# Kernel tuning notes

Hardware: AMD Instinct MI355X
Metric: run time of the kernel (lower is better)

Reference implementation:

```python
import jax, jax.numpy as jnp
import numpy as np

U, I, G = 200000, 100000, 10000
D = 64
LAYERS = 3
E_HG = 3_000_000
E_GI = 2_000_000
B = 8192


def setup_inputs() -> dict:
    key = jax.random.key(0)
    ks = jax.random.split(key, 20)
    n_hg = U + G
    n_gi = G + I
    xav = lambda k, shape: (jax.random.normal(k, shape, jnp.float32) * 0.05)
    inp = {
        "user_inputs": jax.random.randint(ks[0], (B,), 0, U),
        "pos_groups": jax.random.randint(ks[1], (B,), 0, G),
        "neg_groups": jax.random.randint(ks[2], (B,), 0, G),
        # hypergraph propagation matrix (normalized-adjacency-like values)
        "hg_rows": jax.random.randint(ks[3], (E_HG,), 0, n_hg),
        "hg_cols": jax.random.randint(ks[4], (E_HG,), 0, n_hg),
        "hg_vals": jax.random.uniform(ks[5], (E_HG,), jnp.float32) / 16.0,
        # group-item bipartite graph (one LightGCN hop)
        "gi_rows": jax.random.randint(ks[6], (E_GI,), 0, n_gi),
        "gi_cols": jax.random.randint(ks[7], (E_GI,), 0, n_gi),
        "gi_vals": jax.random.uniform(ks[8], (E_GI,), jnp.float32) / 16.0,
        # dense group-group overlap matrix
        "gg_graph": jax.random.uniform(ks[9], (G, G), jnp.float32) / float(G),
        # learned parameters
        "user_emb": xav(ks[10], (U, D)),
        "item_emb": xav(ks[11], (I, D)),
        "group_emb": xav(ks[12], (G, D)),
        "hyper_w": xav(ks[13], (D, 1)),
        "hyper_b": jnp.zeros((1,), jnp.float32),
        "lightgcn_w": xav(ks[14], (D, 1)),
        "lightgcn_b": jnp.zeros((1,), jnp.float32),
        "overlap_w": xav(ks[15], (D, 1)),
        "overlap_b": jnp.zeros((1,), jnp.float32),
    }
    return inp


def spmm(rows, cols, vals, x, n):
    # sparse(n,n) @ x : gather cols, scale, scatter-add into rows
    return jax.ops.segment_sum(vals[:, None] * x[cols], rows, num_segments=n)


def reference(user_inputs, pos_groups, neg_groups,
              hg_rows, hg_cols, hg_vals,
              gi_rows, gi_cols, gi_vals,
              gg_graph,
              user_emb, item_emb, group_emb,
              hyper_w, hyper_b, lightgcn_w, lightgcn_b, overlap_w, overlap_b):
    # --- hypergraph branch: layered SpMM + mean over (layers+1) views ---
    hg = jnp.concatenate([user_emb, group_emb], axis=0)  # [U+G, D]
    acc = hg
    cur = hg
    for _ in range(LAYERS):
        cur = spmm(hg_rows, hg_cols, hg_vals, cur, U + G)
        acc = acc + cur
    hg_mean = acc / float(LAYERS + 1)
    hg_users = hg_mean[:U]   # [U, D]
    hg_groups = hg_mean[U:]  # [G, D]

    # --- lightgcn branch: one SpMM hop over group-item graph ---
    gi = jnp.concatenate([group_emb, item_emb], axis=0)  # [G+I, D]
    gi = spmm(gi_rows, gi_cols, gi_vals, gi, G + I)
    gi_groups = gi[:G]

    # --- overlap branch: dense group-group propagation ---
    gg = gg_graph @ group_emb  # [G, D]

    # --- gated multi-view fusion ---
    sig = jax.nn.sigmoid
    hyper_coef = sig(hg_groups @ hyper_w + hyper_b)      # [G, 1]
    lightgcn_coef = sig(gi_groups @ lightgcn_w + lightgcn_b)
    overlap_coef = sig(gg @ overlap_w + overlap_b)
    groups_final = hyper_coef * hg_groups + lightgcn_coef * gi_groups + overlap_coef * gg
    users_final = hg_users

    return (users_final[user_inputs], groups_final[pos_groups], groups_final[neg_groups],
            user_emb[user_inputs], group_emb[pos_groups], group_emb[neg_groups])
```

## Files before the change

kernel.cpp:

```cpp
#include <hip/hip_runtime.h>
#include <hip/hip_bf16.h>

#define U_N 200000
#define I_N 100000
#define G_N 10000
#define B_N 8192
#define NHG (U_N + G_N)
#define GG_K 10000
#define GG_STRIPES 157
#define GG_SPLIT 8
#define GG_SC_TOT 79
#define GG_KC4 316
#define ROWSTR 136

#define BUCK_SHIFT 8
#define BUCK_ROWS 256
#define NBUCK 821
#define ACHUNK 12288

typedef __attribute__((ext_vector_type(8))) short bf16x8;
typedef __attribute__((ext_vector_type(4))) float f32x4;
typedef __attribute__((ext_vector_type(8))) float f32x8;
typedef __attribute__((ext_vector_type(8))) unsigned short us8;

static __device__ __forceinline__ float sigmoidf_(float x) {
    return 1.0f / (1.0f + __expf(-x));
}

static __device__ __forceinline__ unsigned bfc(float x) {
    unsigned u = __float_as_uint(x);
    return (u + 0x7fffu + ((u >> 16) & 1u)) >> 16;
}
static __device__ __forceinline__ float bsf(unsigned short u) {
    return __uint_as_float((unsigned)u << 16);
}

__global__ void k_phase1(const float* __restrict__ ge, short* __restrict__ Bfrag,
                         int* __restrict__ cursor, int cap, int bfB) {
    int bx = blockIdx.x;
    if (bx < bfB) {
        int t = bx * 256 + threadIdx.x;
        int l = t & 63;
        int ct = (t >> 6) & 3;
        int kc = t >> 8;
        int j = ct * 16 + (l & 15);
        int kb = kc * 32 + (l >> 4) * 8;
        bf16x8 pack;
#pragma unroll
        for (int e = 0; e < 8; ++e) {
            int k = kb + e;
            float f = (k < GG_K) ? ge[(size_t)k * 64 + j] : 0.f;
            pack[e] = (short)bfc(f);
        }
        *(bf16x8*)(Bfrag + (size_t)t * 8) = pack;
        return;
    }
    int b = (bx - bfB) * 256 + threadIdx.x;
    if (b < NBUCK) cursor[b] = b * cap;
}


static __device__ __forceinline__ void bscatter_body(const int* __restrict__ rows,
                                                     const int* __restrict__ cols,
                                                     const float* __restrict__ vals,
                                                     int* __restrict__ cursor,
                                                     int2* __restrict__ bpair,
                                                     int nE, int cap, int blk) {
    __shared__ int h[NBUCK];
    __shared__ int base[NBUCK];
    for (int i = threadIdx.x; i < NBUCK; i += 256) h[i] = 0;
    __syncthreads();
    int s = blk * ACHUNK;
    int end = s + ACHUNK; if (end > nE) end = nE;
    for (int e = s + threadIdx.x; e < end; e += 256)
        atomicAdd(&h[rows[e] >> BUCK_SHIFT], 1);
    __syncthreads();
    for (int i = threadIdx.x; i < NBUCK; i += 256) {
        int c = h[i];
        base[i] = c ? atomicAdd(&cursor[i], c) : 0;
        h[i] = 0;
    }
    __syncthreads();
    for (int e = s + threadIdx.x; e < end; e += 256) {
        int r = rows[e];
        int b = r >> BUCK_SHIFT;
        int pos = base[b] + atomicAdd(&h[b], 1);
        if (pos < (b + 1) * cap)
            bpair[pos] = make_int2(((r & (BUCK_ROWS - 1)) << 24) | cols[e],
                                   __float_as_int(vals[e]));
    }
}

static __device__ __forceinline__ void gg_mfma_body(const float* __restrict__ A,
                                                    const short* __restrict__ Bfrag,
                                                    float* __restrict__ part, int blk) {
    __shared__ short lds_a[64 * ROWSTR];
    const int stripe = blk % GG_STRIPES;
    const int ks = blk / GG_STRIPES;
    const int sc0 = ks * 10;
    const int sc1 = (ks == 7) ? GG_SC_TOT : sc0 + 10;
    const int tid = threadIdx.x;
    const int w = tid >> 6, l = tid & 63;
    const int r0w = stripe * 64 + w * 16;
    const int srow = tid >> 5;
    const int scol = (tid & 31) * 4;
    f32x4 acc0 = {0.f, 0.f, 0.f, 0.f}, acc1 = acc0, acc2 = acc0, acc3 = acc0;
    for (int sc = sc0; sc < sc1; ++sc) {
        __syncthreads();
#pragma unroll
        for (int pass = 0; pass < 8; ++pass) {
            int rl = pass * 8 + srow;
            int rg = stripe * 64 + rl; if (rg > GG_K - 1) rg = GG_K - 1;
            int kg = sc * 128 + scol;
            float4 a = {0.f, 0.f, 0.f, 0.f};
            if (kg < GG_K) a = *(const float4*)(A + (size_t)rg * GG_K + kg);
            ushort4 o;
            o.x = (unsigned short)bfc(a.x); o.y = (unsigned short)bfc(a.y);
            o.z = (unsigned short)bfc(a.z); o.w = (unsigned short)bfc(a.w);
            *(ushort4*)(lds_a + rl * ROWSTR + scol) = o;
        }
        __syncthreads();
#pragma unroll
        for (int q = 0; q < 4; ++q) {
            int kc = sc * 4 + q;
            bf16x8 af = *(const bf16x8*)(lds_a + (w * 16 + (l & 15)) * ROWSTR
                                         + q * 32 + (l >> 4) * 8);
            const bf16x8* bp = (const bf16x8*)(Bfrag + (size_t)kc * 4 * 64 * 8);
            bf16x8 b0 = bp[0 * 64 + l];
            bf16x8 b1 = bp[1 * 64 + l];
            bf16x8 b2 = bp[2 * 64 + l];
            bf16x8 b3 = bp[3 * 64 + l];
            acc0 = __builtin_amdgcn_mfma_f32_16x16x32_bf16(af, b0, acc0, 0, 0, 0);
            acc1 = __builtin_amdgcn_mfma_f32_16x16x32_bf16(af, b1, acc1, 0, 0, 0);
            acc2 = __builtin_amdgcn_mfma_f32_16x16x32_bf16(af, b2, acc2, 0, 0, 0);
            acc3 = __builtin_amdgcn_mfma_f32_16x16x32_bf16(af, b3, acc3, 0, 0, 0);
        }
    }
    float* po = part + (size_t)ks * GG_K * 64;
    const int orow0 = r0w + (l >> 4) * 4;
    const int ocol = l & 15;
#pragma unroll
    for (int reg = 0; reg < 4; ++reg) {
        int orow = orow0 + reg;
        if (orow < GG_K) {
            float* q = po + (size_t)orow * 64 + ocol;
            q[0]  = acc0[reg];
            q[16] = acc1[reg];
            q[32] = acc2[reg];
            q[48] = acc3[reg];
        }
    }
}

__global__ __launch_bounds__(256) void k_phase2(
    const int* __restrict__ rows, const int* __restrict__ cols,
    const float* __restrict__ vals, int* __restrict__ cursor,
    int2* __restrict__ bpair, int nE, int cap,
    const float* __restrict__ A, const short* __restrict__ Bfrag,
    float* __restrict__ part,
    const float4* __restrict__ ue4, const float4* __restrict__ ge4,
    ushort4* __restrict__ out4, const int* __restrict__ ui,
    float* __restrict__ ua, float* __restrict__ grp_acc, float* __restrict__ gi_out,
    int bsB, int ggB, int cvtB, int uaB, int gaB) {
    int bx = blockIdx.x;
    if (bx < bsB) { bscatter_body(rows, cols, vals, cursor, bpair, nE, cap, bx); return; }
    bx -= bsB;
    if (bx < ggB) { gg_mfma_body(A, Bfrag, part, bx); return; }
    bx -= ggB;
    if (bx < cvtB) {
        int i = bx * 256 + threadIdx.x;
        float4 f = (i < U_N * 16) ? ue4[i] : ge4[i - U_N * 16];
        ushort4 o;
        o.x = (unsigned short)bfc(f.x);
        o.y = (unsigned short)bfc(f.y);
        o.z = (unsigned short)bfc(f.z);
        o.w = (unsigned short)bfc(f.w);
        out4[i] = o;
        return;
    }
    bx -= cvtB;
    if (bx < uaB) {
        int idx = bx * 256 + threadIdx.x;
        int b = idx >> 6, d = idx & 63;
        ua[idx] = ((const float*)ue4)[(size_t)ui[b] * 64 + d];
        return;
    }
    bx -= uaB;
    if (bx < gaB) {
        int idx = bx * 256 + threadIdx.x;
        grp_acc[idx] = ((const float*)ge4)[idx];
        return;
    }
    bx -= gaB;
    int idx = bx * 256 + threadIdx.x;
    gi_out[idx] = 0.f;
}


static __device__ __forceinline__ void bcsr_body(const int* __restrict__ cursor,
                                                 const int2* __restrict__ bpair,
                                                 int2* __restrict__ ep,
                                                 int* __restrict__ rp, int* __restrict__ cnt,
                                                 int cap, int b) {
    __shared__ int hist[256];
    __shared__ int sc[256];
    const int tid = threadIdx.x;
    const int s = b * cap;
    int e_ = cursor[b];
    if (e_ > s + cap) e_ = s + cap;
    hist[tid] = 0;
    __syncthreads();
    for (int i = s + tid; i < e_; i += 256)
        atomicAdd(&hist[((unsigned)bpair[i].x) >> 24], 1);
    __syncthreads();
    int v = hist[tid];
    sc[tid] = v;
    __syncthreads();
    for (int off = 1; off < 256; off <<= 1) {
        int t = (tid >= off) ? sc[tid - off] : 0;
        __syncthreads();
        if (tid >= off) sc[tid] += t;
        __syncthreads();
    }
    int excl = sc[tid] - v;
    int gr = (b << BUCK_SHIFT) + tid;
    if (gr < NHG) { rp[gr] = s + excl; cnt[gr] = v; }
    hist[tid] = excl;
    __syncthreads();
    for (int i = s + tid; i < e_; i += 256) {
        int2 p = bpair[i];
        unsigned pk = (unsigned)p.x;
        int pos = atomicAdd(&hist[pk >> 24], 1);
        ep[s + pos] = make_int2((int)(pk & 0xFFFFFFu), p.y);
    }
}

static __device__ __forceinline__ void gi_body(const int* __restrict__ rows,
                                               const int* __restrict__ cols,
                                               const float* __restrict__ vals,
                                               const float* __restrict__ ge,
                                               const float* __restrict__ ie,
                                               float* __restrict__ out, int nE,
                                               int blk, int nblk) {
    int lane = threadIdx.x & 63;
    long wslot = (long)blk * 4 + (threadIdx.x >> 6);
    const long nslots = (long)nblk * 4;
    for (long base = wslot * 64; base < nE; base += nslots * 64) {
        long e = base + lane;
        int r = (e < nE) ? rows[e] : 0x7fffffff;
        bool ok = (r < G_N);
        int c = 0;
        float v = 0.f;
        if (ok) { c = cols[e]; v = vals[e]; }
        unsigned long long mask = __ballot(ok);
        while (mask) {
            int srcl = __ffsll(mask) - 1;
            mask &= mask - 1;
            int rr = __shfl(r, srcl, 64);
            int cc = __shfl(c, srcl, 64);
            float vv = __shfl(v, srcl, 64);
            const float* sp = (cc < G_N) ? (ge + (size_t)cc * 64) : (ie + (size_t)(cc - G_N) * 64);
            atomicAdd(&out[(size_t)rr * 64 + lane], vv * sp[lane]);
        }
    }
}

__global__ __launch_bounds__(256) void k_phase3(const int* __restrict__ cursor,
                                                const int2* __restrict__ bpair,
                                                int2* __restrict__ ep,
                                                int* __restrict__ rp, int* __restrict__ cnt,
                                                int cap,
                                                const int* __restrict__ grows,
                                                const int* __restrict__ gcols,
                                                const float* __restrict__ gvals,
                                                const float* __restrict__ ge,
                                                const float* __restrict__ ie,
                                                float* __restrict__ gi_out, int gnE, int giB) {
    if (blockIdx.x < NBUCK)
        bcsr_body(cursor, bpair, ep, rp, cnt, cap, blockIdx.x);
    else
        gi_body(grows, gcols, gvals, ge, ie, gi_out, gnE, blockIdx.x - NBUCK, giB);
}


static __device__ __forceinline__ void spmm_row8(const int2* __restrict__ ep, int s, int n,
                                                 const us8* __restrict__ x16,
                                                 int sub, f32x8& acc) {
#pragma unroll
    for (int t = 0; t < 8; ++t) acc[t] = 0.f;
    for (int i = 0; i < n; i += 8) {
        int2 e[8];
#pragma unroll
        for (int j = 0; j < 8; ++j) {
            int k = i + j;
            int kk = (k < n) ? k : n - 1;
            e[j] = ep[s + kk];
            if (k >= n) { e[j].y = 0; e[j].x = 0; }
        }
        us8 xv[8];
#pragma unroll
        for (int j = 0; j < 8; ++j)
            xv[j] = x16[(size_t)e[j].x * 8 + sub];
#pragma unroll
        for (int j = 0; j < 8; ++j) {
            float v = __int_as_float(e[j].y);
#pragma unroll
            for (int t = 0; t < 8; ++t) acc[t] += v * bsf(xv[j][t]);
        }
    }
}

__global__ void k_spmm8(const int* __restrict__ rp, const int* __restrict__ cnt,
                        const int2* __restrict__ ep, const us8* __restrict__ x16,
                        us8* __restrict__ out16, float* __restrict__ grp_acc,
                        const int* __restrict__ ui, float* __restrict__ usr_acc,
                        int spmmBlocks) {
    if (blockIdx.x >= spmmBlocks) {
        int idx = (blockIdx.x - spmmBlocks) * 256 + threadIdx.x;
        int b = idx >> 3, d = idx & 7;
        us8 u = x16[(size_t)ui[b] * 8 + d];
        f32x8* g = (f32x8*)usr_acc + ((size_t)b * 8 + d);
        f32x8 t = *g;
#pragma unroll
        for (int j = 0; j < 8; ++j) t[j] += bsf(u[j]);
        *g = t;
        return;
    }
    int wid = threadIdx.x >> 6;
    int lane = threadIdx.x & 63;
    int slot = lane >> 3, sub = lane & 7;
    int r = blockIdx.x * 32 + wid * 8 + slot;
    bool active = (r < NHG);
    int rr = active ? r : NHG - 1;
    int s = rp[rr];
    int n = active ? cnt[rr] : 0;
    f32x8 a;
    spmm_row8(ep, s, n, x16, sub, a);
    if (active) {
        us8 o;
#pragma unroll
        for (int j = 0; j < 8; ++j) o[j] = (unsigned short)bfc(a[j]);
        out16[(size_t)r * 8 + sub] = o;
        if (r >= U_N) {
            f32x8* g = (f32x8*)grp_acc + ((size_t)(r - U_N) * 8 + sub);
            f32x8 t = *g;
#pragma unroll
            for (int j = 0; j < 8; ++j) t[j] += a[j];
            *g = t;
        }
    }
}

__global__ void k_spmm8_final(const int* __restrict__ rp, const int* __restrict__ cnt,
                              const int2* __restrict__ ep, const us8* __restrict__ x16,
                              const int* __restrict__ ui,
                              float* __restrict__ grp_acc, float* __restrict__ usr_acc,
                              int taskBlocks) {
    if (blockIdx.x >= taskBlocks) {
        int idx = (blockIdx.x - taskBlocks) * 256 + threadIdx.x;
        int b = idx >> 3, d = idx & 7;
        us8 u = x16[(size_t)ui[b] * 8 + d];
        f32x8* g = (f32x8*)usr_acc + ((size_t)b * 8 + d);
        f32x8 t = *g;
#pragma unroll
        for (int j = 0; j < 8; ++j) t[j] += bsf(u[j]);
        *g = t;
        return;
    }
    int wid = threadIdx.x >> 6;
    int lane = threadIdx.x & 63;
    int slot = lane >> 3, sub = lane & 7;
    int t = blockIdx.x * 32 + wid * 8 + slot;
    bool active = (t < G_N + B_N);
    int tt = active ? t : 0;
    int r = (tt < G_N) ? (U_N + tt) : ui[tt - G_N];
    int s = rp[r];
    int n = active ? cnt[r] : 0;
    f32x8 a;
    spmm_row8(ep, s, n, x16, sub, a);
    if (active) {
        f32x8* g = (tt < G_N) ? ((f32x8*)grp_acc + ((size_t)tt * 8 + sub))
                              : ((f32x8*)usr_acc + ((size_t)(tt - G_N) * 8 + sub));
        f32x8 v = *g;
#pragma unroll
        for (int j = 0; j < 8; ++j) v[j] += a[j];
        *g = v;
    }
}


__global__ void k_gather_fin(const int* __restrict__ ui, const int* __restrict__ pg,
                             const int* __restrict__ ng, const float* __restrict__ ua,
                             const float* __restrict__ ga, const float* __restrict__ gi_out,
                             const float* __restrict__ gg_part,
                             const float* __restrict__ hw, const float* __restrict__ hb,
                             const float* __restrict__ lw, const float* __restrict__ lb,
                             const float* __restrict__ ow, const float* __restrict__ ob,
                             const float* __restrict__ ue, const float* __restrict__ ge,
                             float* __restrict__ out) {
    int wid = threadIdx.x >> 6, lane = threadIdx.x & 63;
    int b = blockIdx.x * 4 + wid;
    const int S = B_N * 64;
    int u = ui[b], p = pg[b], q = ng[b];
    int idx = b * 64 + lane;
    out[idx]         = ua[idx] * 0.25f;
    out[3 * S + idx] = ue[(size_t)u * 64 + lane];
    out[4 * S + idx] = ge[(size_t)p * 64 + lane];
    out[5 * S + idx] = ge[(size_t)q * 64 + lane];
    const size_t SS = (size_t)G_N * 64;
    float hwv = hw[lane], lwv = lw[lane], owv = ow[lane];
    float hb0 = hb[0], lb0 = lb[0], ob0 = ob[0];
#pragma unroll
    for (int which = 0; which < 2; ++which) {
        int g = which ? q : p;
        size_t o = (size_t)g * 64 + lane;
        float hgv = ga[o] * 0.25f;
        float giv = gi_out[o];
        float ggv = 0.f;
#pragma unroll
        for (int k = 0; k < GG_SPLIT; ++k) ggv += gg_part[k * SS + o];
        float d1 = hgv * hwv, d2 = giv * lwv, d3 = ggv * owv;
#pragma unroll
        for (int off2 = 32; off2; off2 >>= 1) {
            d1 += __shfl_xor(d1, off2, 64);
            d2 += __shfl_xor(d2, off2, 64);
            d3 += __shfl_xor(d3, off2, 64);
        }
        float val = sigmoidf_(d1 + hb0) * hgv + sigmoidf_(d2 + lb0) * giv
                  + sigmoidf_(d3 + ob0) * ggv;
        out[(which ? 2 * S : S) + idx] = val;
    }
}

extern "C" void kernel_launch(void* const* d_in, const int* in_sizes, int n_in,
                              void* d_out, int out_size, void* d_ws, size_t ws_size,
                              hipStream_t stream) {
    const int*   ui        = (const int*)d_in[0];
    const int*   pg        = (const int*)d_in[1];
    const int*   ng        = (const int*)d_in[2];
    const int*   hg_rows   = (const int*)d_in[3];
    const int*   hg_cols   = (const int*)d_in[4];
    const float* hg_vals   = (const float*)d_in[5];
    const int*   gi_rows   = (const int*)d_in[6];
    const int*   gi_cols   = (const int*)d_in[7];
    const float* gi_vals   = (const float*)d_in[8];
    const float* gg_graph  = (const float*)d_in[9];
    const float* user_emb  = (const float*)d_in[10];
    const float* item_emb  = (const float*)d_in[11];
    const float* group_emb = (const float*)d_in[12];
    const float* hyper_w   = (const float*)d_in[13];
    const float* hyper_b   = (const float*)d_in[14];
    const float* lgcn_w    = (const float*)d_in[15];
    const float* lgcn_b    = (const float*)d_in[16];
    const float* ovl_w     = (const float*)d_in[17];
    const float* ovl_b     = (const float*)d_in[18];
    const int E_HG = in_sizes[3];
    const int E_GI = in_sizes[6];

    const int nblkA = (E_HG + ACHUNK - 1) / ACHUNK;
    int cap = (E_HG + NBUCK - 1) / NBUCK;
    cap = cap + cap / 4 + 64;
    cap = (cap + 63) & ~63;

    char* ws = (char*)d_ws;
    size_t off = 0;
    auto alloc = [&](size_t bytes) -> char* {
        char* p = ws + off;
        off += (bytes + 255) & ~(size_t)255;
        return p;
    };
    int*   cursor  = (int*)alloc((size_t)NBUCK * 4);
    int2*  bpair   = (int2*)alloc((size_t)NBUCK * cap * 8);
    int2*  ep      = (int2*)alloc((size_t)NBUCK * cap * 8 + 1024);
    int*   rp      = (int*)alloc((size_t)NHG * 4);
    int*   cnt     = (int*)alloc((size_t)NHG * 4);
    __hip_bfloat16* curA = (__hip_bfloat16*)alloc((size_t)NHG * 64 * 2);
    __hip_bfloat16* curB = (__hip_bfloat16*)alloc((size_t)NHG * 64 * 2);
    float* grp_acc = (float*)alloc((size_t)G_N * 64 * 4);
    float* gi_out  = (float*)alloc((size_t)G_N * 64 * 4);
    float* usr_acc = (float*)alloc((size_t)B_N * 64 * 4);
    short* Bfrag   = (short*)alloc((size_t)GG_KC4 * 4 * 64 * 8 * 2);
    float* gg_part = (float*)alloc((size_t)GG_SPLIT * GG_K * 64 * 4);
    (void)ws_size; (void)n_in; (void)out_size;

    k_phase1<<<GG_KC4 + 4, 256, 0, stream>>>(group_emb, Bfrag, cursor, cap, GG_KC4);

    const int ggB  = GG_STRIPES * GG_SPLIT;
    const int cvtB = (NHG * 16) / 256;
    const int uaB  = (B_N * 64) / 256;
    const int gaB  = (G_N * 64) / 256;
    const int gzB  = (G_N * 64) / 256;
    k_phase2<<<nblkA + ggB + cvtB + uaB + gaB + gzB, 256, 0, stream>>>(
        hg_rows, hg_cols, hg_vals, cursor, bpair, E_HG, cap,
        gg_graph, Bfrag, gg_part,
        (const float4*)user_emb, (const float4*)group_emb, (ushort4*)curB, ui,
        usr_acc, grp_acc, gi_out, nblkA, ggB, cvtB, uaB, gaB);

    const int giB = 2048;
    k_phase3<<<NBUCK + giB, 256, 0, stream>>>(cursor, bpair, ep, rp, cnt, cap,
                                              gi_rows, gi_cols, gi_vals,
                                              group_emb, item_emb, gi_out, E_GI, giB);

    const int spmmB = (NHG + 31) / 32;
    const int uaExt = (B_N * 8) / 256;

    k_spmm8<<<spmmB, 256, 0, stream>>>(rp, cnt, ep, (const us8*)curB,
                                       (us8*)curA, grp_acc, nullptr, nullptr, spmmB);
    k_spmm8<<<spmmB + uaExt, 256, 0, stream>>>(rp, cnt, ep, (const us8*)curA,
                                               (us8*)curB, grp_acc, ui, usr_acc, spmmB);
    const int taskB = (G_N + B_N + 31) / 32;
    k_spmm8_final<<<taskB + uaExt, 256, 0, stream>>>(rp, cnt, ep, (const us8*)curB, ui,
                                                     grp_acc, usr_acc, taskB);

    k_gather_fin<<<B_N / 4, 256, 0, stream>>>(ui, pg, ng, usr_acc, grp_acc, gi_out, gg_part,
                                              hyper_w, hyper_b, lgcn_w, lgcn_b, ovl_w, ovl_b,
                                              user_emb, group_emb, (float*)d_out);
}
```

Before: 395.1 us.

## Move group-item SpMM into phase2, split GEMM K finer, prefetch A tiles

The group-item SpMM blocks move out of phase3 and into the phase2 launch, so they run alongside the bucket scatter and the dense GEMM. Phase3 now does only the CSR build, and zeroing gi_out moves earlier into phase1 so it is done before phase2 adds into it. The dense gg GEMM splits K into 16 pieces instead of 8, giving more blocks, and it prefetches the next A tile into registers while the MFMAs run on the current one. The cost is twice the partial-sum buffer and reduction work in the final gather, plus higher register pressure from the prefetch.

```diff
diff --git a/kernel.cpp b/kernel.cpp
--- a/kernel.cpp
+++ b/kernel.cpp
@@ -8,7 +8,7 @@
 #define NHG (U_N + G_N)
 #define GG_K 10000
 #define GG_STRIPES 157
-#define GG_SPLIT 8
+#define GG_SPLIT 16
 #define GG_SC_TOT 79
 #define GG_KC4 316
 #define ROWSTR 136
@@ -36,7 +36,8 @@
 }
 
 __global__ void k_phase1(const float* __restrict__ ge, short* __restrict__ Bfrag,
-                         int* __restrict__ cursor, int cap, int bfB) {
+                         float* __restrict__ gi_out, int* __restrict__ cursor,
+                         int cap, int bfB, int gzB) {
     int bx = blockIdx.x;
     if (bx < bfB) {
         int t = bx * 256 + threadIdx.x;
@@ -55,7 +56,14 @@
         *(bf16x8*)(Bfrag + (size_t)t * 8) = pack;
         return;
     }
-    int b = (bx - bfB) * 256 + threadIdx.x;
+    bx -= bfB;
+    if (bx < gzB) {
+        int idx = bx * 256 + threadIdx.x;
+        gi_out[idx] = 0.f;
+        return;
+    }
+    bx -= gzB;
+    int b = bx * 256 + threadIdx.x;
     if (b < NBUCK) cursor[b] = b * cap;
 }
 
@@ -97,29 +105,51 @@
     __shared__ short lds_a[64 * ROWSTR];
     const int stripe = blk % GG_STRIPES;
     const int ks = blk / GG_STRIPES;
-    const int sc0 = ks * 10;
-    const int sc1 = (ks == 7) ? GG_SC_TOT : sc0 + 10;
+    const int sc0 = ks * 5;
+    int sc1 = sc0 + 5; if (sc1 > GG_SC_TOT) sc1 = GG_SC_TOT;
     const int tid = threadIdx.x;
     const int w = tid >> 6, l = tid & 63;
     const int r0w = stripe * 64 + w * 16;
     const int srow = tid >> 5;
     const int scol = (tid & 31) * 4;
     f32x4 acc0 = {0.f, 0.f, 0.f, 0.f}, acc1 = acc0, acc2 = acc0, acc3 = acc0;
+    float4 pre[8];
+    int rg_[8];
+#pragma unroll
+    for (int pass = 0; pass < 8; ++pass) {
+        int rg = stripe * 64 + pass * 8 + srow;
+        rg_[pass] = (rg > GG_K - 1) ? GG_K - 1 : rg;
+    }
+    {
+        int kg = sc0 * 128 + scol;
+        bool ok = (kg < GG_K);
+#pragma unroll
+        for (int pass = 0; pass < 8; ++pass) {
+            float4 a = {0.f, 0.f, 0.f, 0.f};
+            if (ok) a = *(const float4*)(A + (size_t)rg_[pass] * GG_K + kg);
+            pre[pass] = a;
+        }
+    }
     for (int sc = sc0; sc < sc1; ++sc) {
         __syncthreads();
 #pragma unroll
         for (int pass = 0; pass < 8; ++pass) {
-            int rl = pass * 8 + srow;
-            int rg = stripe * 64 + rl; if (rg > GG_K - 1) rg = GG_K - 1;
-            int kg = sc * 128 + scol;
-            float4 a = {0.f, 0.f, 0.f, 0.f};
-            if (kg < GG_K) a = *(const float4*)(A + (size_t)rg * GG_K + kg);
             ushort4 o;
-            o.x = (unsigned short)bfc(a.x); o.y = (unsigned short)bfc(a.y);
-            o.z = (unsigned short)bfc(a.z); o.w = (unsigned short)bfc(a.w);
-            *(ushort4*)(lds_a + rl * ROWSTR + scol) = o;
+            o.x = (unsigned short)bfc(pre[pass].x); o.y = (unsigned short)bfc(pre[pass].y);
+            o.z = (unsigned short)bfc(pre[pass].z); o.w = (unsigned short)bfc(pre[pass].w);
+            *(ushort4*)(lds_a + (pass * 8 + srow) * ROWSTR + scol) = o;
         }
         __syncthreads();
+        if (sc + 1 < sc1) {
+            int kg = (sc + 1) * 128 + scol;
+            bool ok = (kg < GG_K);
+#pragma unroll
+            for (int pass = 0; pass < 8; ++pass) {
+                float4 a = {0.f, 0.f, 0.f, 0.f};
+                if (ok) a = *(const float4*)(A + (size_t)rg_[pass] * GG_K + kg);
+                pre[pass] = a;
+            }
+        }
 #pragma unroll
         for (int q = 0; q < 4; ++q) {
             int kc = sc * 4 + q;
@@ -149,89 +179,6 @@
             q[32] = acc2[reg];
             q[48] = acc3[reg];
         }
-    }
-}
-
-__global__ __launch_bounds__(256) void k_phase2(
-    const int* __restrict__ rows, const int* __restrict__ cols,
-    const float* __restrict__ vals, int* __restrict__ cursor,
-    int2* __restrict__ bpair, int nE, int cap,
-    const float* __restrict__ A, const short* __restrict__ Bfrag,
-    float* __restrict__ part,
-    const float4* __restrict__ ue4, const float4* __restrict__ ge4,
-    ushort4* __restrict__ out4, const int* __restrict__ ui,
-    float* __restrict__ ua, float* __restrict__ grp_acc, float* __restrict__ gi_out,
-    int bsB, int ggB, int cvtB, int uaB, int gaB) {
-    int bx = blockIdx.x;
-    if (bx < bsB) { bscatter_body(rows, cols, vals, cursor, bpair, nE, cap, bx); return; }
-    bx -= bsB;
-    if (bx < ggB) { gg_mfma_body(A, Bfrag, part, bx); return; }
-    bx -= ggB;
-    if (bx < cvtB) {
-        int i = bx * 256 + threadIdx.x;
-        float4 f = (i < U_N * 16) ? ue4[i] : ge4[i - U_N * 16];
-        ushort4 o;
-        o.x = (unsigned short)bfc(f.x);
-        o.y = (unsigned short)bfc(f.y);
-        o.z = (unsigned short)bfc(f.z);
-        o.w = (unsigned short)bfc(f.w);
-        out4[i] = o;
-        return;
-    }
-    bx -= cvtB;
-    if (bx < uaB) {
-        int idx = bx * 256 + threadIdx.x;
-        int b = idx >> 6, d = idx & 63;
-        ua[idx] = ((const float*)ue4)[(size_t)ui[b] * 64 + d];
-        return;
-    }
-    bx -= uaB;
-    if (bx < gaB) {
-        int idx = bx * 256 + threadIdx.x;
-        grp_acc[idx] = ((const float*)ge4)[idx];
-        return;
-    }
-    bx -= gaB;
-    int idx = bx * 256 + threadIdx.x;
-    gi_out[idx] = 0.f;
-}
-
-
-static __device__ __forceinline__ void bcsr_body(const int* __restrict__ cursor,
-                                                 const int2* __restrict__ bpair,
-                                                 int2* __restrict__ ep,
-                                                 int* __restrict__ rp, int* __restrict__ cnt,
-                                                 int cap, int b) {
-    __shared__ int hist[256];
-    __shared__ int sc[256];
-    const int tid = threadIdx.x;
-    const int s = b * cap;
-    int e_ = cursor[b];
-    if (e_ > s + cap) e_ = s + cap;
-    hist[tid] = 0;
-    __syncthreads();
-    for (int i = s + tid; i < e_; i += 256)
-        atomicAdd(&hist[((unsigned)bpair[i].x) >> 24], 1);
-    __syncthreads();
-    int v = hist[tid];
-    sc[tid] = v;
-    __syncthreads();
-    for (int off = 1; off < 256; off <<= 1) {
-        int t = (tid >= off) ? sc[tid - off] : 0;
-        __syncthreads();
-        if (tid >= off) sc[tid] += t;
-        __syncthreads();
-    }
-    int excl = sc[tid] - v;
-    int gr = (b << BUCK_SHIFT) + tid;
-    if (gr < NHG) { rp[gr] = s + excl; cnt[gr] = v; }
-    hist[tid] = excl;
-    __syncthreads();
-    for (int i = s + tid; i < e_; i += 256) {
-        int2 p = bpair[i];
-        unsigned pk = (unsigned)p.x;
-        int pos = atomicAdd(&hist[pk >> 24], 1);
-        ep[s + pos] = make_int2((int)(pk & 0xFFFFFFu), p.y);
     }
 }
 
@@ -265,21 +212,90 @@
     }
 }
 
+__global__ __launch_bounds__(256) void k_phase2(
+    const int* __restrict__ rows, const int* __restrict__ cols,
+    const float* __restrict__ vals, int* __restrict__ cursor,
+    int2* __restrict__ bpair, int nE, int cap,
+    const float* __restrict__ A, const short* __restrict__ Bfrag,
+    float* __restrict__ part,
+    const int* __restrict__ grows, const int* __restrict__ gcols,
+    const float* __restrict__ gvals, const float* __restrict__ ie,
+    float* __restrict__ gi_out, int gnE,
+    const float4* __restrict__ ue4, const float4* __restrict__ ge4,
+    ushort4* __restrict__ out4, const int* __restrict__ ui,
+    float* __restrict__ ua, float* __restrict__ grp_acc,
+    int bsB, int ggB, int giB, int cvtB, int uaB) {
+    int bx = blockIdx.x;
+    if (bx < bsB) { bscatter_body(rows, cols, vals, cursor, bpair, nE, cap, bx); return; }
+    bx -= bsB;
+    if (bx < ggB) { gg_mfma_body(A, Bfrag, part, bx); return; }
+    bx -= ggB;
+    if (bx < giB) {
+        gi_body(grows, gcols, gvals, (const float*)ge4, ie, gi_out, gnE, bx, giB);
+        return;
+    }
+    bx -= giB;
+    if (bx < cvtB) {
+        int i = bx * 256 + threadIdx.x;
+        float4 f = (i < U_N * 16) ? ue4[i] : ge4[i - U_N * 16];
+        ushort4 o;
+        o.x = (unsigned short)bfc(f.x);
+        o.y = (unsigned short)bfc(f.y);
+        o.z = (unsigned short)bfc(f.z);
+        o.w = (unsigned short)bfc(f.w);
+        out4[i] = o;
+        return;
+    }
+    bx -= cvtB;
+    if (bx < uaB) {
+        int idx = bx * 256 + threadIdx.x;
+        int b = idx >> 6, d = idx & 63;
+        ua[idx] = ((const float*)ue4)[(size_t)ui[b] * 64 + d];
+        return;
+    }
+    bx -= uaB;
+    int idx = bx * 256 + threadIdx.x;
+    grp_acc[idx] = ((const float*)ge4)[idx];
+}
+
+
 __global__ __launch_bounds__(256) void k_phase3(const int* __restrict__ cursor,
                                                 const int2* __restrict__ bpair,
                                                 int2* __restrict__ ep,
                                                 int* __restrict__ rp, int* __restrict__ cnt,
-                                                int cap,
-                                                const int* __restrict__ grows,
-                                                const int* __restrict__ gcols,
-                                                const float* __restrict__ gvals,
-                                                const float* __restrict__ ge,
-                                                const float* __restrict__ ie,
-                                                float* __restrict__ gi_out, int gnE, int giB) {
-    if (blockIdx.x < NBUCK)
-        bcsr_body(cursor, bpair, ep, rp, cnt, cap, blockIdx.x);
-    else
-        gi_body(grows, gcols, gvals, ge, ie, gi_out, gnE, blockIdx.x - NBUCK, giB);
+                                                int cap) {
+    __shared__ int hist[256];
+    __shared__ int sc[256];
+    const int b = blockIdx.x;
+    const int tid = threadIdx.x;
+    const int s = b * cap;
+    int e_ = cursor[b];
+    if (e_ > s + cap) e_ = s + cap;
+    hist[tid] = 0;
+    __syncthreads();
+    for (int i = s + tid; i < e_; i += 256)
+        atomicAdd(&hist[((unsigned)bpair[i].x) >> 24], 1);
+    __syncthreads();
+    int v = hist[tid];
+    sc[tid] = v;
+    __syncthreads();
+    for (int off = 1; off < 256; off <<= 1) {
+        int t = (tid >= off) ? sc[tid - off] : 0;
+        __syncthreads();
+        if (tid >= off) sc[tid] += t;
+        __syncthreads();
+    }
+    int excl = sc[tid] - v;
+    int gr = (b << BUCK_SHIFT) + tid;
+    if (gr < NHG) { rp[gr] = s + excl; cnt[gr] = v; }
+    hist[tid] = excl;
+    __syncthreads();
+    for (int i = s + tid; i < e_; i += 256) {
+        int2 p = bpair[i];
+        unsigned pk = (unsigned)p.x;
+        int pos = atomicAdd(&hist[pk >> 24], 1);
+        ep[s + pos] = make_int2((int)(pk & 0xFFFFFFu), p.y);
+    }
 }
 
 
@@ -483,23 +499,23 @@
     float* gg_part = (float*)alloc((size_t)GG_SPLIT * GG_K * 64 * 4);
     (void)ws_size; (void)n_in; (void)out_size;
 
-    k_phase1<<<GG_KC4 + 4, 256, 0, stream>>>(group_emb, Bfrag, cursor, cap, GG_KC4);
+    const int gzB = (G_N * 64) / 256;
+    k_phase1<<<GG_KC4 + gzB + 4, 256, 0, stream>>>(group_emb, Bfrag, gi_out, cursor,
+                                                   cap, GG_KC4, gzB);
 
     const int ggB  = GG_STRIPES * GG_SPLIT;
+    const int giB  = 1536;
     const int cvtB = (NHG * 16) / 256;
     const int uaB  = (B_N * 64) / 256;
     const int gaB  = (G_N * 64) / 256;
-    const int gzB  = (G_N * 64) / 256;
-    k_phase2<<<nblkA + ggB + cvtB + uaB + gaB + gzB, 256, 0, stream>>>(
+    k_phase2<<<nblkA + ggB + giB + cvtB + uaB + gaB, 256, 0, stream>>>(
         hg_rows, hg_cols, hg_vals, cursor, bpair, E_HG, cap,
         gg_graph, Bfrag, gg_part,
+        gi_rows, gi_cols, gi_vals, item_emb, gi_out, E_GI,
         (const float4*)user_emb, (const float4*)group_emb, (ushort4*)curB, ui,
-        usr_acc, grp_acc, gi_out, nblkA, ggB, cvtB, uaB, gaB);
-
-    const int giB = 2048;
-    k_phase3<<<NBUCK + giB, 256, 0, stream>>>(cursor, bpair, ep, rp, cnt, cap,
-                                              gi_rows, gi_cols, gi_vals,
-                                              group_emb, item_emb, gi_out, E_GI, giB);
+        usr_acc, grp_acc, nblkA, ggB, giB, cvtB, uaB);
+
+    k_phase3<<<NBUCK, 256, 0, stream>>>(cursor, bpair, ep, rp, cnt, cap);
 
     const int spmmB = (NHG + 31) / 32;
     const int uaExt = (B_N * 8) / 256;
```

Result: slower. 403.9 us (+2.2%).
